# Kernel tuning notes

Hardware: AMD Instinct MI355X
Metric: run time of the kernel (lower is better)

Reference implementation:

```python
import jax, jax.numpy as jnp
import numpy as np

B, S1, S2 = 4, 2048, 2048
IN1, IN2 = 512, 512
KD, VD, H = 64, 64, 8


def setup_inputs() -> dict:
    key = jax.random.key(0)
    ks = jax.random.split(key, 7)
    x1 = jax.random.normal(ks[0], (B, S1, IN1), dtype=jnp.float32)
    x2 = jax.random.normal(ks[1], (B, S2, IN2), dtype=jnp.float32)
    # nn.Linear weights stored as [out, in]; kaiming-uniform-ish scale
    Wq = jax.random.normal(ks[2], (KD * H, IN1), dtype=jnp.float32) * (1.0 / np.sqrt(IN1))
    Wk = jax.random.normal(ks[3], (KD * H, IN2), dtype=jnp.float32) * (1.0 / np.sqrt(IN2))
    Wv = jax.random.normal(ks[4], (VD * H, IN2), dtype=jnp.float32) * (1.0 / np.sqrt(IN2))
    Wo = jax.random.normal(ks[5], (IN1, VD * H), dtype=jnp.float32) * (1.0 / np.sqrt(VD * H))
    bo = jax.random.normal(ks[6], (IN1,), dtype=jnp.float32) * 0.01
    return {"x1": x1, "x2": x2, "Wq": Wq, "Wk": Wk, "Wv": Wv, "Wo": Wo, "bo": bo}


def reference(x1, x2, Wq, Wk, Wv, Wo, bo):
    b, s1, _ = x1.shape
    s2 = x2.shape[1]
    # projections -> [B, H, S, D]
    q = (x1 @ Wq.T).reshape(b, s1, H, KD).transpose(0, 2, 1, 3)
    k = (x2 @ Wk.T).reshape(b, s2, H, KD).transpose(0, 2, 1, 3)
    v = (x2 @ Wv.T).reshape(b, s2, H, VD).transpose(0, 2, 1, 3)
    # scores [B, H, S1, S2]
    attn = jnp.einsum('bhqd,bhkd->bhqk', q, k) / jnp.sqrt(jnp.float32(KD))
    attn = jax.nn.softmax(attn, axis=-1)
    out = jnp.einsum('bhqk,bhkd->bhqd', attn, v)  # [B, H, S1, VD]
    out = out.transpose(0, 2, 1, 3).reshape(b, s1, H * VD)
    return out @ Wo.T + bo
```

## Files before the change

kernel.cpp:

```cpp
#include <hip/hip_runtime.h>
#include <stdint.h>

typedef __bf16 bf16;
typedef __bf16 bf16x8 __attribute__((ext_vector_type(8)));
typedef __bf16 bf16x4 __attribute__((ext_vector_type(4)));
typedef float f32x4 __attribute__((ext_vector_type(4)));

#define MFMA16x16x32(A, B, C) __builtin_amdgcn_mfma_f32_16x16x32_bf16((A), (B), (C), 0, 0, 0)
#define SBAR() do { __builtin_amdgcn_s_barrier(); __builtin_amdgcn_sched_barrier(0); } while (0)

__device__ __forceinline__ void gload_lds16(const void* g, void* l) {
  __builtin_amdgcn_global_load_lds((const __attribute__((address_space(1))) void*)g,
                                   (__attribute__((address_space(3))) void*)l,
                                   16, 0, 0);
}

__device__ __forceinline__ float fexp2(float x) { return __builtin_amdgcn_exp2f(x); }

__device__ __forceinline__ bf16x8 cvt8(float4 a, float4 b) {
  bf16x8 o;
  o[0] = (bf16)a.x; o[1] = (bf16)a.y; o[2] = (bf16)a.z; o[3] = (bf16)a.w;
  o[4] = (bf16)b.x; o[5] = (bf16)b.y; o[6] = (bf16)b.z; o[7] = (bf16)b.w;
  return o;
}

__global__ void cast_x(const float* __restrict__ x1, const float* __restrict__ x2,
                       bf16* __restrict__ out) {
  const size_t i = ((size_t)blockIdx.x * blockDim.x + threadIdx.x) * 8;
  const float* src = (i < 4194304) ? x1 + i : x2 + (i - 4194304);
  float4 a = *reinterpret_cast<const float4*>(src);
  float4 b = *reinterpret_cast<const float4*>(src + 4);
  *reinterpret_cast<bf16x8*>(out + i) = cvt8(a, b);
}

template <int MODE>
__global__ __launch_bounds__(256, 4) void proj_kernel(
    const bf16* __restrict__ A0, const bf16* __restrict__ A1,
    const float* __restrict__ W0, const float* __restrict__ W1,
    const float* __restrict__ W2, void* __restrict__ C0, void* __restrict__ C1,
    void* __restrict__ C2, const float* __restrict__ bias) {
  __shared__ bf16 As[3][128 * 32];
  __shared__ bf16 Bs[2][64 * 32];
  const int tid = threadIdx.x;
  const int w = tid >> 6, l = tid & 63;
  const int wr = w >> 1, wc = w & 1;
  const int lr = l & 15, lg = l >> 4;
  const int bm = blockIdx.x, bn = blockIdx.y;
  const int K = 512;

  int sel = 0, wn = bn;
  const bf16* A;
  const float* Bf;
  if constexpr (MODE == 0) {
    sel = bn >> 3;
    wn = bn & 7;
    A = (sel == 0) ? A0 : A1;
    Bf = ((sel == 0) ? W0 : (sel == 1) ? W1 : W2) + (size_t)wn * 64 * K;
  } else {
    A = A0;
    Bf = W0 + (size_t)bn * 64 * K;
  }

  const int c_row = l >> 2;
  const int c_s = l & 3;
  const int sw = (c_s ^ (c_row & 3)) * 8;

  float4 lb[2][2];
  auto issue_A = [&](int t, int bb) {
#pragma unroll
    for (int i = 0; i < 2; i++) {
      const int q = w + i * 4;
      gload_lds16(A + (size_t)(bm * 128 + q * 16 + c_row) * K + t * 32 + sw, &As[bb][q * 512]);
    }
  };
  auto issue_B = [&](int t, int s) {
    const float* pb = Bf + (size_t)(w * 16 + c_row) * K + t * 32 + c_s * 8;
    lb[s][0] = *reinterpret_cast<const float4*>(pb);
    lb[s][1] = *reinterpret_cast<const float4*>(pb + 4);
  };
  auto commit_B = [&](int s, int bb) {
    *reinterpret_cast<bf16x8*>(&Bs[bb][w * 512 + c_row * 32 + sw]) = cvt8(lb[s][0], lb[s][1]);
  };

  f32x4 acc[4][2] = {};
  const int swz = (lr & 3) * 8;

  issue_A(0, 0); issue_B(0, 0);
  issue_A(1, 1); issue_B(1, 1);
  asm volatile("s_waitcnt vmcnt(4)" ::: "memory");
  commit_B(0, 0);
  asm volatile("s_waitcnt lgkmcnt(0)" ::: "memory");
  SBAR();

  const int NT = 16;
  for (int t = 0; t < NT; t++) {
    if (t + 2 < NT) { issue_A(t + 2, (t + 2) % 3); issue_B(t + 2, t & 1); }

    bf16x8 a[4], b[2];
    const int cur = t % 3;
#pragma unroll
    for (int mi = 0; mi < 4; mi++)
      a[mi] = *reinterpret_cast<const bf16x8*>(
          &As[cur][(wr * 64 + mi * 16 + lr) * 32 + (lg * 8 ^ swz)]);
#pragma unroll
    for (int ni = 0; ni < 2; ni++)
      b[ni] = *reinterpret_cast<const bf16x8*>(
          &Bs[t & 1][(wc * 32 + ni * 16 + lr) * 32 + (lg * 8 ^ swz)]);
#pragma unroll
    for (int mi = 0; mi < 4; mi++)
#pragma unroll
      for (int ni = 0; ni < 2; ni++)
        acc[mi][ni] = MFMA16x16x32(a[mi], b[ni], acc[mi][ni]);

    if (t + 1 < NT) {
      if (t + 2 < NT) asm volatile("s_waitcnt vmcnt(4)" ::: "memory");
      else            asm volatile("s_waitcnt vmcnt(0)" ::: "memory");
      commit_B((t + 1) & 1, (t + 1) & 1);
      asm volatile("s_waitcnt lgkmcnt(0)" ::: "memory");
      SBAR();
    }
  }

#pragma unroll
  for (int mi = 0; mi < 4; mi++) {
    const int m0 = bm * 128 + wr * 64 + mi * 16 + lg * 4;
#pragma unroll
    for (int ni = 0; ni < 2; ni++) {
      const int n = wc * 32 + ni * 16 + lr;
      if constexpr (MODE == 0) {
        const int gn = wn * 64 + n;
        if (sel < 2) {
          bf16* dst = (bf16*)((sel == 0) ? C0 : C1);
          const float scale = (sel == 0) ? 0.18033688011112f : 1.0f;
#pragma unroll
          for (int r = 0; r < 4; r++) {
            const int m = m0 + r;
            size_t d = (size_t)((m >> 11) * 8 + (gn >> 6)) * 131072 + (size_t)(m & 2047) * 64 + (gn & 63);
            dst[d] = (bf16)(acc[mi][ni][r] * scale);
          }
        } else {
          bf16x4 pv;
#pragma unroll
          for (int r = 0; r < 4; r++) pv[r] = (bf16)acc[mi][ni][r];
          size_t base = ((size_t)(m0 >> 11) * 512 + gn) * 2048 + (m0 & 2047);
          *reinterpret_cast<bf16x4*>((bf16*)C2 + base) = pv;
        }
      } else {
        const int gn = bn * 64 + n;
        const float bv = bias[gn];
#pragma unroll
        for (int r = 0; r < 4; r++)
          ((float*)C0)[(size_t)(m0 + r) * 512 + gn] = acc[mi][ni][r] + bv;
      }
    }
  }
}

__global__ __launch_bounds__(256, 2) void attn_kernel(
    const bf16* __restrict__ Q, const bf16* __restrict__ Kk,
    const bf16* __restrict__ Vt, bf16* __restrict__ AO) {
  __shared__ bf16 Kb2[3][64 * 64];
  __shared__ bf16 Vb2[3][64 * 64];
  __shared__ bf16 Ps[4][32 * 64];

  const int tid = threadIdx.x;
  const int w = tid >> 6, l = tid & 63;
  const int lr = l & 15, lg = l >> 4;

  const int lin = blockIdx.x;
  const int xcd = lin & 7;
  const int m = lin >> 3;
  const int bh = xcd * 4 + (m & 3);
  const int qb = m >> 2;
  const int b = bh >> 3, h = bh & 7;

  const bf16* Qb = Q + (size_t)bh * 131072;
  const bf16* Kb = Kk + (size_t)bh * 131072;
  const bf16* Vb = Vt + (size_t)bh * 131072;

  const int q0 = qb * 128 + w * 32;

  bf16x8 qf[2][2];
#pragma unroll
  for (int i = 0; i < 2; i++)
#pragma unroll
    for (int ks = 0; ks < 2; ks++)
      qf[i][ks] = *reinterpret_cast<const bf16x8*>(
          Qb + (size_t)(q0 + i * 16 + lr) * 64 + ks * 32 + lg * 8);

  const int crow = l >> 3;
  const int scol = ((l & 7) ^ crow) * 8;
  auto stage = [&](int kv0, int bb) {
#pragma unroll
    for (int i = 0; i < 2; i++) {
      const int ch = w * 2 + i;
      const int row = ch * 8 + crow;
      gload_lds16(Kb + (size_t)(kv0 + row) * 64 + scol, &Kb2[bb][ch * 512]);
      gload_lds16(Vb + (size_t)row * 2048 + kv0 + scol, &Vb2[bb][ch * 512]);
    }
  };

  f32x4 oacc[2][4] = {};
  float lsum[2] = {0.f, 0.f};
  const int sw8 = (lr & 7) * 8;

  stage(0, 0);
  stage(64, 1);
  asm volatile("s_waitcnt vmcnt(4)" ::: "memory");
  SBAR();

  for (int t = 0; t < 32; t++) {
    const int cur = t % 3;
    if (t + 2 < 32) stage((t + 2) * 64, (t + 2) % 3);

    bf16x8 kb[2][4];
#pragma unroll
    for (int ks = 0; ks < 2; ks++)
#pragma unroll
      for (int c = 0; c < 4; c++)
        kb[ks][c] = *reinterpret_cast<const bf16x8*>(
            &Kb2[cur][(c * 16 + lr) * 64 + ((ks * 32 + lg * 8) ^ sw8)]);

#pragma unroll
    for (int i = 0; i < 2; i++) {
      f32x4 st[4] = {};
#pragma unroll
      for (int ks = 0; ks < 2; ks++)
#pragma unroll
        for (int c = 0; c < 4; c++)
          st[c] = MFMA16x16x32(kb[ks][c], qf[i][ks], st[c]);
#pragma unroll
      for (int c = 0; c < 4; c++) {
        float e0 = fexp2(st[c][0]);
        float e1 = fexp2(st[c][1]);
        float e2 = fexp2(st[c][2]);
        float e3 = fexp2(st[c][3]);
        lsum[i] += (e0 + e1) + (e2 + e3);
        bf16x4 pk;
        pk[0] = (bf16)e0; pk[1] = (bf16)e1; pk[2] = (bf16)e2; pk[3] = (bf16)e3;
        *reinterpret_cast<bf16x4*>(
            &Ps[w][(i * 16 + lr) * 64 + ((c * 16 + lg * 4) ^ sw8)]) = pk;
      }
    }

    bf16x8 vb[2][4];
#pragma unroll
    for (int ks = 0; ks < 2; ks++)
#pragma unroll
      for (int c = 0; c < 4; c++)
        vb[ks][c] = *reinterpret_cast<const bf16x8*>(
            &Vb2[cur][(c * 16 + lr) * 64 + ((ks * 32 + lg * 8) ^ sw8)]);

#pragma unroll
    for (int i = 0; i < 2; i++)
#pragma unroll
      for (int ks = 0; ks < 2; ks++) {
        bf16x8 pa = *reinterpret_cast<const bf16x8*>(
            &Ps[w][(i * 16 + lr) * 64 + ((ks * 32 + lg * 8) ^ sw8)]);
#pragma unroll
        for (int c = 0; c < 4; c++)
          oacc[i][c] = MFMA16x16x32(pa, vb[ks][c], oacc[i][c]);
      }

    if (t < 30)       asm volatile("s_waitcnt vmcnt(4) lgkmcnt(0)" ::: "memory");
    else if (t == 30) asm volatile("s_waitcnt vmcnt(0) lgkmcnt(0)" ::: "memory");
    if (t < 31) SBAR();
  }

#pragma unroll
  for (int i = 0; i < 2; i++) {
    lsum[i] += __shfl_xor(lsum[i], 16);
    lsum[i] += __shfl_xor(lsum[i], 32);
  }

#pragma unroll
  for (int i = 0; i < 2; i++) {
#pragma unroll
    for (int r = 0; r < 4; r++) {
      const float inv = 1.f / __shfl(lsum[i], lg * 4 + r);
      const int qrow = q0 + i * 16 + lg * 4 + r;
#pragma unroll
      for (int c = 0; c < 4; c++)
        AO[(size_t)(b * 2048 + qrow) * 512 + h * 64 + c * 16 + lr] = (bf16)(oacc[i][c][r] * inv);
    }
  }
}

extern "C" void kernel_launch(void* const* d_in, const int* in_sizes, int n_in,
                              void* d_out, int out_size, void* d_ws, size_t ws_size,
                              hipStream_t stream) {
  (void)in_sizes; (void)n_in; (void)out_size; (void)ws_size;
  const float* x1 = (const float*)d_in[0];
  const float* x2 = (const float*)d_in[1];
  const float* Wq = (const float*)d_in[2];
  const float* Wk = (const float*)d_in[3];
  const float* Wv = (const float*)d_in[4];
  const float* Wo = (const float*)d_in[5];
  const float* bo = (const float*)d_in[6];

  uint8_t* ws = (uint8_t*)d_ws;
  bf16* x1b = (bf16*)(ws + 0);
  bf16* x2b = (bf16*)(ws + 8388608);
  bf16* AO  = (bf16*)(ws + 0);
  bf16* Qws = (bf16*)(ws + 16777216);
  bf16* Kws = (bf16*)(ws + 25165824);
  bf16* Vtw = (bf16*)(ws + 33554432);

  cast_x<<<4096, 256, 0, stream>>>(x1, x2, x1b);

  proj_kernel<0><<<dim3(64, 24), 256, 0, stream>>>(x1b, x2b, Wq, Wk, Wv, Qws, Kws, Vtw, nullptr);

  attn_kernel<<<512, 256, 0, stream>>>(Qws, Kws, Vtw, AO);

  proj_kernel<1><<<dim3(64, 8), 256, 0, stream>>>(AO, nullptr, Wo, nullptr, nullptr, d_out, nullptr, nullptr, bo);
}
```

Measured before the change: 103.2 us.

## Use 32x32x16 MFMA in attention and keep P in registers via permlane swap

Switches the attention kernel from 16x16x32 to 32x32x16 bf16 MFMA, computing S^T per wave so the exponentiated scores can be packed with v_cvt_pk_bf16_f32 and redistributed with v_permlane32_swap. This lets the P operand feed the PV MFMA directly, removing the per-wave LDS P buffer with its stores, loads and LDS traffic. K and V fragment reads are restructured for the new layout and the output normalisation is rewritten for the 32x32 accumulator layout. The risks are higher register pressure from 16-wide accumulators and correctness of the permlane-based operand layout.

Result: no change. 103.1 us (-0.1%).

```diff
diff --git a/kernel.cpp b/kernel.cpp
--- a/kernel.cpp
+++ b/kernel.cpp
@@ -5,8 +5,11 @@
 typedef __bf16 bf16x8 __attribute__((ext_vector_type(8)));
 typedef __bf16 bf16x4 __attribute__((ext_vector_type(4)));
 typedef float f32x4 __attribute__((ext_vector_type(4)));
+typedef float f32x16 __attribute__((ext_vector_type(16)));
+typedef uint32_t u32x4 __attribute__((ext_vector_type(4)));
 
 #define MFMA16x16x32(A, B, C) __builtin_amdgcn_mfma_f32_16x16x32_bf16((A), (B), (C), 0, 0, 0)
+#define MFMA32x32x16(A, B, C) __builtin_amdgcn_mfma_f32_32x32x16_bf16((A), (B), (C), 0, 0, 0)
 #define SBAR() do { __builtin_amdgcn_s_barrier(); __builtin_amdgcn_sched_barrier(0); } while (0)
 
 __device__ __forceinline__ void gload_lds16(const void* g, void* l) {
@@ -16,6 +19,15 @@
 }
 
 __device__ __forceinline__ float fexp2(float x) { return __builtin_amdgcn_exp2f(x); }
+
+__device__ __forceinline__ uint32_t cvtpk(float a, float b) {
+  uint32_t r;
+  asm("v_cvt_pk_bf16_f32 %0, %1, %2" : "=v"(r) : "v"(a), "v"(b));
+  return r;
+}
+__device__ __forceinline__ void plswap(uint32_t& a, uint32_t& b) {
+  asm volatile("v_permlane32_swap_b32 %0, %1" : "+v"(a), "+v"(b));
+}
 
 __device__ __forceinline__ bf16x8 cvt8(float4 a, float4 b) {
   bf16x8 o;
@@ -161,18 +173,18 @@
     const bf16* __restrict__ Vt, bf16* __restrict__ AO) {
   __shared__ bf16 Kb2[3][64 * 64];
   __shared__ bf16 Vb2[3][64 * 64];
-  __shared__ bf16 Ps[4][32 * 64];
 
   const int tid = threadIdx.x;
   const int w = tid >> 6, l = tid & 63;
-  const int lr = l & 15, lg = l >> 4;
+  const int q32 = l & 31;
+  const int h = l >> 5;
 
   const int lin = blockIdx.x;
   const int xcd = lin & 7;
   const int m = lin >> 3;
   const int bh = xcd * 4 + (m & 3);
   const int qb = m >> 2;
-  const int b = bh >> 3, h = bh & 7;
+  const int b = bh >> 3, hd = bh & 7;
 
   const bf16* Qb = Q + (size_t)bh * 131072;
   const bf16* Kb = Kk + (size_t)bh * 131072;
@@ -180,13 +192,11 @@
 
   const int q0 = qb * 128 + w * 32;
 
-  bf16x8 qf[2][2];
-#pragma unroll
-  for (int i = 0; i < 2; i++)
-#pragma unroll
-    for (int ks = 0; ks < 2; ks++)
-      qf[i][ks] = *reinterpret_cast<const bf16x8*>(
-          Qb + (size_t)(q0 + i * 16 + lr) * 64 + ks * 32 + lg * 8);
+  bf16x8 qf[4];
+#pragma unroll
+  for (int ks = 0; ks < 4; ks++)
+    qf[ks] = *reinterpret_cast<const bf16x8*>(
+        Qb + (size_t)(q0 + q32) * 64 + ks * 16 + h * 8);
 
   const int crow = l >> 3;
   const int scol = ((l & 7) ^ crow) * 8;
@@ -200,9 +210,9 @@
     }
   };
 
-  f32x4 oacc[2][4] = {};
-  float lsum[2] = {0.f, 0.f};
-  const int sw8 = (lr & 7) * 8;
+  f32x16 oacc[2] = {};
+  float lsum = 0.f;
+  const int l7 = l & 7;
 
   stage(0, 0);
   stage(64, 1);
@@ -213,75 +223,67 @@
     const int cur = t % 3;
     if (t + 2 < 32) stage((t + 2) * 64, (t + 2) % 3);
 
-    bf16x8 kb[2][4];
-#pragma unroll
-    for (int ks = 0; ks < 2; ks++)
-#pragma unroll
-      for (int c = 0; c < 4; c++)
-        kb[ks][c] = *reinterpret_cast<const bf16x8*>(
-            &Kb2[cur][(c * 16 + lr) * 64 + ((ks * 32 + lg * 8) ^ sw8)]);
-
-#pragma unroll
-    for (int i = 0; i < 2; i++) {
-      f32x4 st[4] = {};
-#pragma unroll
-      for (int ks = 0; ks < 2; ks++)
-#pragma unroll
-        for (int c = 0; c < 4; c++)
-          st[c] = MFMA16x16x32(kb[ks][c], qf[i][ks], st[c]);
-#pragma unroll
-      for (int c = 0; c < 4; c++) {
-        float e0 = fexp2(st[c][0]);
-        float e1 = fexp2(st[c][1]);
-        float e2 = fexp2(st[c][2]);
-        float e3 = fexp2(st[c][3]);
-        lsum[i] += (e0 + e1) + (e2 + e3);
-        bf16x4 pk;
-        pk[0] = (bf16)e0; pk[1] = (bf16)e1; pk[2] = (bf16)e2; pk[3] = (bf16)e3;
-        *reinterpret_cast<bf16x4*>(
-            &Ps[w][(i * 16 + lr) * 64 + ((c * 16 + lg * 4) ^ sw8)]) = pk;
+#pragma unroll
+    for (int rb = 0; rb < 2; rb++) {
+      bf16x8 kb[4];
+#pragma unroll
+      for (int ks = 0; ks < 4; ks++)
+        kb[ks] = *reinterpret_cast<const bf16x8*>(
+            &Kb2[cur][(rb * 32 + q32) * 64 + (((ks * 2 + h) ^ l7) * 8)]);
+
+      f32x16 st = {};
+#pragma unroll
+      for (int ks = 0; ks < 4; ks++)
+        st = MFMA32x32x16(kb[ks], qf[ks], st);
+
+      float e[16];
+#pragma unroll
+      for (int r = 0; r < 16; r++) {
+        e[r] = fexp2(st[r]);
+        lsum += e[r];
       }
-    }
-
-    bf16x8 vb[2][4];
-#pragma unroll
-    for (int ks = 0; ks < 2; ks++)
-#pragma unroll
-      for (int c = 0; c < 4; c++)
-        vb[ks][c] = *reinterpret_cast<const bf16x8*>(
-            &Vb2[cur][(c * 16 + lr) * 64 + ((ks * 32 + lg * 8) ^ sw8)]);
-
-#pragma unroll
-    for (int i = 0; i < 2; i++)
-#pragma unroll
-      for (int ks = 0; ks < 2; ks++) {
-        bf16x8 pa = *reinterpret_cast<const bf16x8*>(
-            &Ps[w][(i * 16 + lr) * 64 + ((ks * 32 + lg * 8) ^ sw8)]);
-#pragma unroll
-        for (int c = 0; c < 4; c++)
-          oacc[i][c] = MFMA16x16x32(pa, vb[ks][c], oacc[i][c]);
+      uint32_t Qp[8];
+#pragma unroll
+      for (int p = 0; p < 8; p++) Qp[p] = cvtpk(e[2 * p], e[2 * p + 1]);
+      plswap(Qp[0], Qp[2]);
+      plswap(Qp[1], Qp[3]);
+      plswap(Qp[4], Qp[6]);
+      plswap(Qp[5], Qp[7]);
+      const bf16x8 pa0 = __builtin_bit_cast(bf16x8, (u32x4){Qp[0], Qp[1], Qp[2], Qp[3]});
+      const bf16x8 pa1 = __builtin_bit_cast(bf16x8, (u32x4){Qp[4], Qp[5], Qp[6], Qp[7]});
+
+#pragma unroll
+      for (int kst = 0; kst < 2; kst++) {
+        const bf16x8 pa = (kst == 0) ? pa0 : pa1;
+#pragma unroll
+        for (int db = 0; db < 2; db++) {
+          bf16x8 vb = *reinterpret_cast<const bf16x8*>(
+              &Vb2[cur][(db * 32 + q32) * 64 + (((rb * 4 + kst * 2 + h) ^ l7) * 8)]);
+          oacc[db] = MFMA32x32x16(pa, vb, oacc[db]);
+        }
       }
+    }
 
     if (t < 30)       asm volatile("s_waitcnt vmcnt(4) lgkmcnt(0)" ::: "memory");
     else if (t == 30) asm volatile("s_waitcnt vmcnt(0) lgkmcnt(0)" ::: "memory");
     if (t < 31) SBAR();
   }
 
-#pragma unroll
-  for (int i = 0; i < 2; i++) {
-    lsum[i] += __shfl_xor(lsum[i], 16);
-    lsum[i] += __shfl_xor(lsum[i], 32);
-  }
-
-#pragma unroll
-  for (int i = 0; i < 2; i++) {
-#pragma unroll
-    for (int r = 0; r < 4; r++) {
-      const float inv = 1.f / __shfl(lsum[i], lg * 4 + r);
-      const int qrow = q0 + i * 16 + lg * 4 + r;
-#pragma unroll
-      for (int c = 0; c < 4; c++)
-        AO[(size_t)(b * 2048 + qrow) * 512 + h * 64 + c * 16 + lr] = (bf16)(oacc[i][c][r] * inv);
+  lsum += __shfl_xor(lsum, 32);
+
+  float inv[16];
+#pragma unroll
+  for (int r = 0; r < 16; r++) {
+    const int qv = (r & 3) + 8 * (r >> 2) + 4 * h;
+    inv[r] = 1.f / __shfl(lsum, qv);
+  }
+#pragma unroll
+  for (int db = 0; db < 2; db++) {
+#pragma unroll
+    for (int r = 0; r < 16; r++) {
+      const int qv = (r & 3) + 8 * (r >> 2) + 4 * h;
+      AO[(size_t)(b * 2048 + q0 + qv) * 512 + hd * 64 + db * 32 + q32] =
+          (bf16)(oacc[db][r] * inv[r]);
     }
   }
 }
```
